# Kernel tuning notes

Measured on AMD Instinct MI355X. Metric: run time of the kernel, lower is better.

## Reference

```python
import jax, jax.numpy as jnp
import numpy as np

N_NODES = 100000
N_EDGES = 1600000
IN_DIM = 128
OUT_DIM = 16
HEADS = 4
NEG_SLOPE = 0.2


def setup_inputs() -> dict:
    key = jax.random.key(0)
    k1, k2, k3, k4, k5, k6, k7 = jax.random.split(key, 7)
    feat = jax.random.normal(k1, (N_NODES, IN_DIM), dtype=jnp.float32)
    src = jax.random.randint(k2, (N_EDGES,), 0, N_NODES, dtype=jnp.int32)
    dst = jax.random.randint(k3, (N_EDGES,), 0, N_NODES, dtype=jnp.int32)
    # Xavier-ish init for learned params (as in dgl GATConv)
    W = jax.random.normal(k4, (IN_DIM, HEADS * OUT_DIM), dtype=jnp.float32) / np.sqrt(IN_DIM)
    attn_l = jax.random.normal(k5, (HEADS, OUT_DIM), dtype=jnp.float32) / np.sqrt(OUT_DIM)
    attn_r = jax.random.normal(k6, (HEADS, OUT_DIM), dtype=jnp.float32) / np.sqrt(OUT_DIM)
    bias = jnp.zeros((HEADS * OUT_DIM,), dtype=jnp.float32)
    return {"feat": feat, "W": W, "attn_l": attn_l, "attn_r": attn_r,
            "bias": bias, "src": src, "dst": dst}


def reference(feat, W, attn_l, attn_r, bias, src, dst):
    N = feat.shape[0]
    H, D = attn_l.shape
    # Linear projection: [N, H, D]
    h = (feat @ W).reshape(N, H, D)
    # Per-node attention halves: [N, H]
    el = jnp.sum(h * attn_l[None], axis=-1)
    er = jnp.sum(h * attn_r[None], axis=-1)
    # Per-edge logits with LeakyReLU: [E, H]
    e = jax.nn.leaky_relu(el[src] + er[dst], negative_slope=NEG_SLOPE)
    # Segment softmax over incoming edges of each destination node
    e_max = jax.ops.segment_max(e, dst, num_segments=N)  # [N, H]
    ex = jnp.exp(e - e_max[dst])
    denom = jax.ops.segment_sum(ex, dst, num_segments=N)  # [N, H]
    alpha = ex / denom[dst]  # [E, H]
    # Scatter-weighted aggregation of source features
    msg = h[src] * alpha[:, :, None]  # [E, H, D]
    out = jax.ops.segment_sum(msg, dst, num_segments=N)  # [N, H, D]
    return out + bias.reshape(1, H, D)
```

## Files before the change

### kernel.cpp

```cpp
#include <hip/hip_runtime.h>
#include <math.h>

#define N_NODES 100000
#define N_EDGES 1600000
#define IN_DIM  128
#define HD      64
#define HEADS   4
#define ODIM    16
#define NEG_SLOPE 0.2f

#define BSH 8
#define NB  ((N_NODES + 255) >> 8)
#define PART_BLOCKS 256
#define EPB ((N_EDGES + PART_BLOCKS - 1) / PART_BLOCKS)
#define MAT (NB * PART_BLOCKS)
#define CAP 12288

__device__ inline unsigned short f32_to_bf16_rne(float f) {
    unsigned int b = __float_as_uint(f);
    b += 0x7FFFu + ((b >> 16) & 1u);
    return (unsigned short)(b >> 16);
}
__device__ inline float bf16_to_f32(unsigned short u) {
    return __uint_as_float(((unsigned int)u) << 16);
}

__global__ __launch_bounds__(256) void k_gemm_fused(const float* __restrict__ feat,
                                                    const float* __restrict__ W,
                                                    const float* __restrict__ attn_l,
                                                    const float* __restrict__ attn_r,
                                                    unsigned short* __restrict__ hbf,
                                                    float* __restrict__ el,
                                                    float* __restrict__ er) {
    __shared__ float sFT[32][132];
    __shared__ float sW[32][64];

    const int tid  = threadIdx.x;
    const int nid  = tid >> 4;
    const int cid  = tid & 15;
    const int c0   = cid * 4;
    const int nblk = blockIdx.x * 128;

    const int ln  = tid & 127;
    const int lkq = tid >> 7;

    float acc[8][4] = {};

    for (int kc = 0; kc < 4; ++kc) {
        const int k0 = kc * 32;
        const int gn = nblk + ln;
        #pragma unroll
        for (int i = 0; i < 4; ++i) {
            float4 v = (gn < N_NODES)
                ? *(const float4*)&feat[(size_t)gn * IN_DIM + k0 + lkq * 16 + i * 4]
                : make_float4(0.f, 0.f, 0.f, 0.f);
            const int kk = lkq * 16 + i * 4;
            sFT[kk + 0][ln] = v.x;
            sFT[kk + 1][ln] = v.y;
            sFT[kk + 2][ln] = v.z;
            sFT[kk + 3][ln] = v.w;
        }
        {
            const float4* W4 = (const float4*)(W + k0 * HD);
            float4 a = W4[tid];
            float4 b = W4[tid + 256];
            ((float4*)&sW[0][0])[tid]       = a;
            ((float4*)&sW[0][0])[tid + 256] = b;
        }
        __syncthreads();

        #pragma unroll 8
        for (int k = 0; k < 32; ++k) {
            float4 w  = *(const float4*)&sW[k][c0];
            float4 fA = *(const float4*)&sFT[k][nid * 8];
            float4 fB = *(const float4*)&sFT[k][nid * 8 + 4];
            float fr[8] = {fA.x, fA.y, fA.z, fA.w, fB.x, fB.y, fB.z, fB.w};
            #pragma unroll
            for (int r = 0; r < 8; ++r) {
                acc[r][0] = fmaf(fr[r], w.x, acc[r][0]);
                acc[r][1] = fmaf(fr[r], w.y, acc[r][1]);
                acc[r][2] = fmaf(fr[r], w.z, acc[r][2]);
                acc[r][3] = fmaf(fr[r], w.w, acc[r][3]);
            }
        }
        __syncthreads();
    }

    float4 al = *(const float4*)&attn_l[c0];
    float4 ar = *(const float4*)&attn_r[c0];
    const int head = cid >> 2;
    #pragma unroll
    for (int r = 0; r < 8; ++r) {
        int gn = nblk + nid * 8 + r;
        float pl = acc[r][0]*al.x + acc[r][1]*al.y + acc[r][2]*al.z + acc[r][3]*al.w;
        float pr = acc[r][0]*ar.x + acc[r][1]*ar.y + acc[r][2]*ar.z + acc[r][3]*ar.w;
        pl += __shfl_xor(pl, 1); pl += __shfl_xor(pl, 2);
        pr += __shfl_xor(pr, 1); pr += __shfl_xor(pr, 2);
        if (gn < N_NODES) {
            ushort4 hv;
            hv.x = f32_to_bf16_rne(acc[r][0]);
            hv.y = f32_to_bf16_rne(acc[r][1]);
            hv.z = f32_to_bf16_rne(acc[r][2]);
            hv.w = f32_to_bf16_rne(acc[r][3]);
            *(ushort4*)&hbf[(size_t)gn * HD + c0] = hv;
            if ((cid & 3) == 0) {
                el[gn * HEADS + head] = pl;
                er[gn * HEADS + head] = pr;
            }
        }
    }
}

__global__ __launch_bounds__(256) void k_count(const int* __restrict__ dst,
                                               int* __restrict__ counts) {
    __shared__ int h[NB];
    for (int i = threadIdx.x; i < NB; i += 256) h[i] = 0;
    __syncthreads();
    int beg = blockIdx.x * EPB;
    int end = beg + EPB; if (end > N_EDGES) end = N_EDGES;
    for (int e = beg + threadIdx.x; e < end; e += 256)
        atomicAdd(&h[dst[e] >> BSH], 1);
    __syncthreads();
    for (int i = threadIdx.x; i < NB; i += 256)
        counts[i * PART_BLOCKS + blockIdx.x] = h[i];
}

__global__ __launch_bounds__(256) void k_scanA(int* __restrict__ counts,
                                               int* __restrict__ bsums) {
    __shared__ int wsum[4];
    const int t = threadIdx.x;
    const int i = blockIdx.x * 256 + t;
    const int lane = t & 63, wv = t >> 6;
    int v = counts[i];
    int x = v;
    #pragma unroll
    for (int o = 1; o < 64; o <<= 1) {
        int u = __shfl_up(x, o);
        if (lane >= o) x += u;
    }
    if (lane == 63) wsum[wv] = x;
    __syncthreads();
    if (t == 0) {
        int r = 0;
        #pragma unroll
        for (int w = 0; w < 4; ++w) { int u = wsum[w]; wsum[w] = r; r += u; }
    }
    __syncthreads();
    int excl = x - v + wsum[wv];
    counts[i] = excl;
    if (t == 255) bsums[blockIdx.x] = excl + v;
}

__global__ __launch_bounds__(512) void k_scanB(int* __restrict__ bsums) {
    __shared__ int s[512];
    const int t = threadIdx.x;
    int v = (t < NB) ? bsums[t] : 0;
    s[t] = v;
    __syncthreads();
    for (int o = 1; o < 512; o <<= 1) {
        int u = (t >= o) ? s[t - o] : 0;
        __syncthreads();
        s[t] += u;
        __syncthreads();
    }
    if (t < NB) bsums[t] = s[t] - v;
}

__global__ __launch_bounds__(256) void k_partition(const int* __restrict__ src,
                                                   const int* __restrict__ dst,
                                                   const int* __restrict__ offs,
                                                   const int* __restrict__ bsums,
                                                   int* __restrict__ edges) {
    __shared__ int cur[NB];
    for (int i = threadIdx.x; i < NB; i += 256)
        cur[i] = offs[i * PART_BLOCKS + blockIdx.x] + bsums[i];
    __syncthreads();
    int beg = blockIdx.x * EPB;
    int end = beg + EPB; if (end > N_EDGES) end = N_EDGES;
    for (int e = beg + threadIdx.x; e < end; e += 256) {
        int d = dst[e];
        int pos = atomicAdd(&cur[d >> BSH], 1);
        edges[pos] = (int)(((unsigned)(d & 255) << 24) | (unsigned)src[e]);
    }
}

__global__ __launch_bounds__(256) void k_bucket_sort(const int* __restrict__ bsums,
                                                     int* __restrict__ edges,
                                                     int* __restrict__ deg_g,
                                                     int* __restrict__ cend_g) {
    __shared__ int stage[CAP];
    __shared__ int cnt[256];
    __shared__ int pos[256];
    __shared__ int wsum[4];
    const int b = blockIdx.x;
    const int t = threadIdx.x;
    const int base = bsums[b];
    const int bend = (b + 1 < NB) ? bsums[b + 1] : N_EDGES;
    int n = bend - base;
    if (n > CAP) n = CAP;

    for (int i = t; i < n; i += 256) stage[i] = edges[base + i];
    cnt[t] = 0;
    __syncthreads();
    for (int i = t; i < n; i += 256)
        atomicAdd(&cnt[((unsigned)stage[i]) >> 24], 1);
    __syncthreads();

    const int lane = t & 63, wv = t >> 6;
    int v = cnt[t];
    int x = v;
    #pragma unroll
    for (int o = 1; o < 64; o <<= 1) {
        int u = __shfl_up(x, o);
        if (lane >= o) x += u;
    }
    if (lane == 63) wsum[wv] = x;
    __syncthreads();
    if (t == 0) {
        int r = 0;
        #pragma unroll
        for (int w = 0; w < 4; ++w) { int u = wsum[w]; wsum[w] = r; r += u; }
    }
    __syncthreads();
    int excl = x - v + wsum[wv];
    pos[t] = excl;
    int node = (b << 8) + t;
    if (node < N_NODES) {
        deg_g[node]  = v;
        cend_g[node] = base + excl + v;
    }
    __syncthreads();

    for (int i = t; i < n; i += 256) {
        int e  = stage[i];
        int p  = atomicAdd(&pos[((unsigned)e) >> 24], 1);
        edges[base + p] = e & 0x00FFFFFF;
    }
}

#define NPW 4
__global__ __launch_bounds__(256) void k_aggregate_csr(
        const int* __restrict__ sorted_src,
        const int* __restrict__ cursor_end,
        const int* __restrict__ deg,
        const unsigned short* __restrict__ hbf,
        const float* __restrict__ el,
        const float* __restrict__ er,
        const float* __restrict__ bias,
        float* __restrict__ out) {
    const int wave = threadIdx.x >> 6;
    const int lane = threadIdx.x & 63;
    const int n0   = (blockIdx.x * 4 + wave) * NPW;
    if (n0 >= N_NODES) return;

    const int h1   = lane & 3;
    const int slot = lane >> 2;
    const int g    = lane >> 5;
    const int c    = lane & 31;
    const int hd   = c >> 3;

    int   endv[NPW], j0[NPW];
    float er1[NPW];
    float l_p[NPW];
    float accL[NPW], accH[NPW];

    #pragma unroll
    for (int k = 0; k < NPW; ++k) {
        int nk = n0 + k;
        bool ok = nk < N_NODES;
        endv[k] = ok ? cursor_end[nk] : 0;
        int dn  = ok ? deg[nk] : 0;
        j0[k]   = endv[k] - dn;
        er1[k]  = ok ? er[nk * HEADS + h1] : 0.f;
        l_p[k] = 0.f;
        accL[k] = 0.f; accH[k] = 0.f;
    }

    for (;;) {
        bool any = false;
        #pragma unroll
        for (int k = 0; k < NPW; ++k) any |= (j0[k] < endv[k]);
        if (!any) break;

        int   sK[NPW];
        float pK[NPW];
        #pragma unroll
        for (int k = 0; k < NPW; ++k) {
            int j = j0[k] + slot;
            sK[k] = (j0[k] < endv[k] && j < endv[k]) ? sorted_src[j] : -1;
        }
        #pragma unroll
        for (int k = 0; k < NPW; ++k) {
            if (sK[k] >= 0) {
                float t = el[sK[k] * HEADS + h1] + er1[k];
                t = t > 0.f ? t : NEG_SLOPE * t;
                pK[k] = __expf(t);
            } else {
                pK[k] = 0.f;
            }
        }
        #pragma unroll
        for (int k = 0; k < NPW; ++k) {
            if (j0[k] >= endv[k]) continue;
            float cs = pK[k];
            cs += __shfl_xor(cs, 4);
            cs += __shfl_xor(cs, 8);
            cs += __shfl_xor(cs, 16);
            cs += __shfl_xor(cs, 32);
            l_p[k] += cs;
        }
        #pragma unroll
        for (int k = 0; k < NPW; ++k) {
            if (j0[k] >= endv[k]) continue;
            float pe[8];
            unsigned off[8];
            #pragma unroll
            for (int t = 0; t < 8; ++t) {
                int e = 2 * t + g;
                pe[t] = __shfl(pK[k], e * 4 + hd);
                int se = __shfl(sK[k], e * 4);
                unsigned row = (se < 0) ? 0u : (unsigned)se;
                off[t] = row * HD + 2 * c;
            }
            unsigned u[8];
            #pragma unroll
            for (int t = 0; t < 8; ++t)
                u[t] = *(const unsigned*)&hbf[off[t]];
            #pragma unroll
            for (int t = 0; t < 8; ++t) {
                accL[k] = fmaf(pe[t], bf16_to_f32((unsigned short)(u[t] & 0xffffu)), accL[k]);
                accH[k] = fmaf(pe[t], bf16_to_f32((unsigned short)(u[t] >> 16)),     accH[k]);
            }
            j0[k] += 16;
        }
    }

    const float2 bl = ((const float2*)bias)[c];
    #pragma unroll
    for (int k = 0; k < NPW; ++k) {
        int nk = n0 + k;
        if (nk >= N_NODES) continue;
        float l   = __shfl(l_p[k], hd);
        float inv = (l > 0.f) ? 1.f / l : 0.f;
        float vL = accL[k] + __shfl_xor(accL[k], 32);
        float vH = accH[k] + __shfl_xor(accH[k], 32);
        if (lane < 32) {
            float2 v = make_float2(vL * inv + bl.x, vH * inv + bl.y);
            *(float2*)&out[nk * HD + 2 * c] = v;
        }
    }
}

extern "C" void kernel_launch(void* const* d_in, const int* in_sizes, int n_in,
                              void* d_out, int out_size, void* d_ws, size_t ws_size,
                              hipStream_t stream) {
    const float* feat   = (const float*)d_in[0];
    const float* W      = (const float*)d_in[1];
    const float* attn_l = (const float*)d_in[2];
    const float* attn_r = (const float*)d_in[3];
    const float* bias   = (const float*)d_in[4];
    const int*   src    = (const int*)d_in[5];
    const int*   dst    = (const int*)d_in[6];
    float* out = (float*)d_out;

    unsigned short* hbf = (unsigned short*)d_ws;
    float* el    = (float*)(hbf + (size_t)N_NODES * HD);
    float* er    = el + (size_t)N_NODES * HEADS;
    int*   deg    = (int*)(er + (size_t)N_NODES * HEADS);
    int*   cend   = deg + N_NODES;
    int*   edges  = cend + N_NODES;
    int*   counts = edges + N_EDGES;
    int*   bsums  = counts + MAT;

    k_gemm_fused<<<(N_NODES + 127) / 128, 256, 0, stream>>>(feat, W, attn_l, attn_r,
                                                            hbf, el, er);
    k_count<<<PART_BLOCKS, 256, 0, stream>>>(dst, counts);
    k_scanA<<<NB, 256, 0, stream>>>(counts, bsums);
    k_scanB<<<1, 512, 0, stream>>>(bsums);
    k_partition<<<PART_BLOCKS, 256, 0, stream>>>(src, dst, counts, bsums, edges);
    k_bucket_sort<<<NB, 256, 0, stream>>>(bsums, edges, deg, cend);
    const int nodes_per_block = 4 * NPW;
    k_aggregate_csr<<<(N_NODES + nodes_per_block - 1) / nodes_per_block, 256, 0, stream>>>(
        edges, cend, deg, hbf, el, er, bias, out);
}
```

Measured before the change: 240.7 us.

## Fuse bucket sort into aggregation and merge count into GEMM launch

```diff
diff --git a/kernel.cpp b/kernel.cpp
--- a/kernel.cpp
+++ b/kernel.cpp
@@ -9,12 +9,13 @@
 #define ODIM    16
 #define NEG_SLOPE 0.2f
 
-#define BSH 8
-#define NB  ((N_NODES + 255) >> 8)
+#define BSH 6
+#define NB  1563
 #define PART_BLOCKS 256
 #define EPB ((N_EDGES + PART_BLOCKS - 1) / PART_BLOCKS)
 #define MAT (NB * PART_BLOCKS)
-#define CAP 12288
+#define CAP2 1536
+#define G_GEMM ((N_NODES + 127) / 128)
 
 __device__ inline unsigned short f32_to_bf16_rne(float f) {
     unsigned int b = __float_as_uint(f);
@@ -25,104 +26,107 @@
     return __uint_as_float(((unsigned int)u) << 16);
 }
 
-__global__ __launch_bounds__(256) void k_gemm_fused(const float* __restrict__ feat,
+__global__ __launch_bounds__(256) void k_gemm_count(const float* __restrict__ feat,
                                                     const float* __restrict__ W,
                                                     const float* __restrict__ attn_l,
                                                     const float* __restrict__ attn_r,
+                                                    const int* __restrict__ dst,
                                                     unsigned short* __restrict__ hbf,
                                                     float* __restrict__ el,
-                                                    float* __restrict__ er) {
-    __shared__ float sFT[32][132];
-    __shared__ float sW[32][64];
-
-    const int tid  = threadIdx.x;
-    const int nid  = tid >> 4;
-    const int cid  = tid & 15;
-    const int c0   = cid * 4;
-    const int nblk = blockIdx.x * 128;
-
-    const int ln  = tid & 127;
-    const int lkq = tid >> 7;
-
-    float acc[8][4] = {};
-
-    for (int kc = 0; kc < 4; ++kc) {
-        const int k0 = kc * 32;
-        const int gn = nblk + ln;
-        #pragma unroll
-        for (int i = 0; i < 4; ++i) {
-            float4 v = (gn < N_NODES)
-                ? *(const float4*)&feat[(size_t)gn * IN_DIM + k0 + lkq * 16 + i * 4]
-                : make_float4(0.f, 0.f, 0.f, 0.f);
-            const int kk = lkq * 16 + i * 4;
-            sFT[kk + 0][ln] = v.x;
-            sFT[kk + 1][ln] = v.y;
-            sFT[kk + 2][ln] = v.z;
-            sFT[kk + 3][ln] = v.w;
-        }
-        {
-            const float4* W4 = (const float4*)(W + k0 * HD);
-            float4 a = W4[tid];
-            float4 b = W4[tid + 256];
-            ((float4*)&sW[0][0])[tid]       = a;
-            ((float4*)&sW[0][0])[tid + 256] = b;
-        }
+                                                    float* __restrict__ er,
+                                                    int* __restrict__ counts) {
+    __shared__ __align__(16) char smem[25088];
+    const int tid = threadIdx.x;
+
+    if (blockIdx.x < G_GEMM) {
+        float (*sFT)[132] = (float (*)[132])smem;
+        float (*sW)[64]   = (float (*)[64])(smem + 16896);
+
+        const int nid  = tid >> 4;
+        const int cid  = tid & 15;
+        const int c0   = cid * 4;
+        const int nblk = blockIdx.x * 128;
+        const int ln   = tid & 127;
+        const int lkq  = tid >> 7;
+
+        float acc[8][4] = {};
+
+        for (int kc = 0; kc < 4; ++kc) {
+            const int k0 = kc * 32;
+            const int gn = nblk + ln;
+            #pragma unroll
+            for (int i = 0; i < 4; ++i) {
+                float4 v = (gn < N_NODES)
+                    ? *(const float4*)&feat[(size_t)gn * IN_DIM + k0 + lkq * 16 + i * 4]
+                    : make_float4(0.f, 0.f, 0.f, 0.f);
+                const int kk = lkq * 16 + i * 4;
+                sFT[kk + 0][ln] = v.x;
+                sFT[kk + 1][ln] = v.y;
+                sFT[kk + 2][ln] = v.z;
+                sFT[kk + 3][ln] = v.w;
+            }
+            {
+                const float4* W4 = (const float4*)(W + k0 * HD);
+                float4 a = W4[tid];
+                float4 b = W4[tid + 256];
+                ((float4*)&sW[0][0])[tid]       = a;
+                ((float4*)&sW[0][0])[tid + 256] = b;
+            }
+            __syncthreads();
+
+            #pragma unroll 8
+            for (int k = 0; k < 32; ++k) {
+                float4 w  = *(const float4*)&sW[k][c0];
+                float4 fA = *(const float4*)&sFT[k][nid * 8];
+                float4 fB = *(const float4*)&sFT[k][nid * 8 + 4];
+                float fr[8] = {fA.x, fA.y, fA.z, fA.w, fB.x, fB.y, fB.z, fB.w};
+                #pragma unroll
+                for (int r = 0; r < 8; ++r) {
+                    acc[r][0] = fmaf(fr[r], w.x, acc[r][0]);
+                    acc[r][1] = fmaf(fr[r], w.y, acc[r][1]);
+                    acc[r][2] = fmaf(fr[r], w.z, acc[r][2]);
+                    acc[r][3] = fmaf(fr[r], w.w, acc[r][3]);
+                }
+            }
+            __syncthreads();
+        }
+
+        float4 al = *(const float4*)&attn_l[c0];
+        float4 ar = *(const float4*)&attn_r[c0];
+        const int head = cid >> 2;
+        #pragma unroll
+        for (int r = 0; r < 8; ++r) {
+            int gn = nblk + nid * 8 + r;
+            float pl = acc[r][0]*al.x + acc[r][1]*al.y + acc[r][2]*al.z + acc[r][3]*al.w;
+            float pr = acc[r][0]*ar.x + acc[r][1]*ar.y + acc[r][2]*ar.z + acc[r][3]*ar.w;
+            pl += __shfl_xor(pl, 1); pl += __shfl_xor(pl, 2);
+            pr += __shfl_xor(pr, 1); pr += __shfl_xor(pr, 2);
+            if (gn < N_NODES) {
+                ushort4 hv;
+                hv.x = f32_to_bf16_rne(acc[r][0]);
+                hv.y = f32_to_bf16_rne(acc[r][1]);
+                hv.z = f32_to_bf16_rne(acc[r][2]);
+                hv.w = f32_to_bf16_rne(acc[r][3]);
+                *(ushort4*)&hbf[(size_t)gn * HD + c0] = hv;
+                if ((cid & 3) == 0) {
+                    el[gn * HEADS + head] = pl;
+                    er[gn * HEADS + head] = pr;
+                }
+            }
+        }
+    } else {
+        int* hcnt = (int*)smem;
+        const int cb = blockIdx.x - G_GEMM;
+        for (int i = tid; i < NB; i += 256) hcnt[i] = 0;
         __syncthreads();
-
-        #pragma unroll 8
-        for (int k = 0; k < 32; ++k) {
-            float4 w  = *(const float4*)&sW[k][c0];
-            float4 fA = *(const float4*)&sFT[k][nid * 8];
-            float4 fB = *(const float4*)&sFT[k][nid * 8 + 4];
-            float fr[8] = {fA.x, fA.y, fA.z, fA.w, fB.x, fB.y, fB.z, fB.w};
-            #pragma unroll
-            for (int r = 0; r < 8; ++r) {
-                acc[r][0] = fmaf(fr[r], w.x, acc[r][0]);
-                acc[r][1] = fmaf(fr[r], w.y, acc[r][1]);
-                acc[r][2] = fmaf(fr[r], w.z, acc[r][2]);
-                acc[r][3] = fmaf(fr[r], w.w, acc[r][3]);
-            }
-        }
+        int beg = cb * EPB;
+        int end = beg + EPB; if (end > N_EDGES) end = N_EDGES;
+        for (int e = beg + tid; e < end; e += 256)
+            atomicAdd(&hcnt[dst[e] >> BSH], 1);
         __syncthreads();
-    }
-
-    float4 al = *(const float4*)&attn_l[c0];
-    float4 ar = *(const float4*)&attn_r[c0];
-    const int head = cid >> 2;
-    #pragma unroll
-    for (int r = 0; r < 8; ++r) {
-        int gn = nblk + nid * 8 + r;
-        float pl = acc[r][0]*al.x + acc[r][1]*al.y + acc[r][2]*al.z + acc[r][3]*al.w;
-        float pr = acc[r][0]*ar.x + acc[r][1]*ar.y + acc[r][2]*ar.z + acc[r][3]*ar.w;
-        pl += __shfl_xor(pl, 1); pl += __shfl_xor(pl, 2);
-        pr += __shfl_xor(pr, 1); pr += __shfl_xor(pr, 2);
-        if (gn < N_NODES) {
-            ushort4 hv;
-            hv.x = f32_to_bf16_rne(acc[r][0]);
-            hv.y = f32_to_bf16_rne(acc[r][1]);
-            hv.z = f32_to_bf16_rne(acc[r][2]);
-            hv.w = f32_to_bf16_rne(acc[r][3]);
-            *(ushort4*)&hbf[(size_t)gn * HD + c0] = hv;
-            if ((cid & 3) == 0) {
-                el[gn * HEADS + head] = pl;
-                er[gn * HEADS + head] = pr;
-            }
-        }
-    }
-}
-
-__global__ __launch_bounds__(256) void k_count(const int* __restrict__ dst,
-                                               int* __restrict__ counts) {
-    __shared__ int h[NB];
-    for (int i = threadIdx.x; i < NB; i += 256) h[i] = 0;
-    __syncthreads();
-    int beg = blockIdx.x * EPB;
-    int end = beg + EPB; if (end > N_EDGES) end = N_EDGES;
-    for (int e = beg + threadIdx.x; e < end; e += 256)
-        atomicAdd(&h[dst[e] >> BSH], 1);
-    __syncthreads();
-    for (int i = threadIdx.x; i < NB; i += 256)
-        counts[i * PART_BLOCKS + blockIdx.x] = h[i];
+        for (int i = tid; i < NB; i += 256)
+            counts[i * PART_BLOCKS + cb] = hcnt[i];
+    }
 }
 
 __global__ __launch_bounds__(256) void k_scanA(int* __restrict__ counts,
@@ -151,19 +155,23 @@
     if (t == 255) bsums[blockIdx.x] = excl + v;
 }
 
-__global__ __launch_bounds__(512) void k_scanB(int* __restrict__ bsums) {
-    __shared__ int s[512];
+__global__ __launch_bounds__(1024) void k_scanB(int* __restrict__ bsums) {
+    __shared__ int s[1024];
     const int t = threadIdx.x;
-    int v = (t < NB) ? bsums[t] : 0;
+    int v0 = (2 * t     < NB) ? bsums[2 * t]     : 0;
+    int v1 = (2 * t + 1 < NB) ? bsums[2 * t + 1] : 0;
+    int v = v0 + v1;
     s[t] = v;
     __syncthreads();
-    for (int o = 1; o < 512; o <<= 1) {
+    for (int o = 1; o < 1024; o <<= 1) {
         int u = (t >= o) ? s[t - o] : 0;
         __syncthreads();
         s[t] += u;
         __syncthreads();
     }
-    if (t < NB) bsums[t] = s[t] - v;
+    int run = s[t] - v;
+    if (2 * t < NB)     bsums[2 * t]     = run;
+    if (2 * t + 1 < NB) bsums[2 * t + 1] = run + v0;
 }
 
 __global__ __launch_bounds__(256) void k_partition(const int* __restrict__ src,
@@ -180,173 +188,154 @@
     for (int e = beg + threadIdx.x; e < end; e += 256) {
         int d = dst[e];
         int pos = atomicAdd(&cur[d >> BSH], 1);
-        edges[pos] = (int)(((unsigned)(d & 255) << 24) | (unsigned)src[e]);
-    }
-}
-
-__global__ __launch_bounds__(256) void k_bucket_sort(const int* __restrict__ bsums,
-                                                     int* __restrict__ edges,
-                                                     int* __restrict__ deg_g,
-                                                     int* __restrict__ cend_g) {
-    __shared__ int stage[CAP];
-    __shared__ int cnt[256];
-    __shared__ int pos[256];
-    __shared__ int wsum[4];
-    const int b = blockIdx.x;
-    const int t = threadIdx.x;
-    const int base = bsums[b];
-    const int bend = (b + 1 < NB) ? bsums[b + 1] : N_EDGES;
-    int n = bend - base;
-    if (n > CAP) n = CAP;
-
-    for (int i = t; i < n; i += 256) stage[i] = edges[base + i];
-    cnt[t] = 0;
-    __syncthreads();
-    for (int i = t; i < n; i += 256)
-        atomicAdd(&cnt[((unsigned)stage[i]) >> 24], 1);
-    __syncthreads();
-
-    const int lane = t & 63, wv = t >> 6;
-    int v = cnt[t];
-    int x = v;
-    #pragma unroll
-    for (int o = 1; o < 64; o <<= 1) {
-        int u = __shfl_up(x, o);
-        if (lane >= o) x += u;
-    }
-    if (lane == 63) wsum[wv] = x;
-    __syncthreads();
-    if (t == 0) {
-        int r = 0;
-        #pragma unroll
-        for (int w = 0; w < 4; ++w) { int u = wsum[w]; wsum[w] = r; r += u; }
-    }
-    __syncthreads();
-    int excl = x - v + wsum[wv];
-    pos[t] = excl;
-    int node = (b << 8) + t;
-    if (node < N_NODES) {
-        deg_g[node]  = v;
-        cend_g[node] = base + excl + v;
-    }
-    __syncthreads();
-
-    for (int i = t; i < n; i += 256) {
-        int e  = stage[i];
-        int p  = atomicAdd(&pos[((unsigned)e) >> 24], 1);
-        edges[base + p] = e & 0x00FFFFFF;
+        edges[pos] = (int)(((unsigned)(d & 63) << 24) | (unsigned)src[e]);
     }
 }
 
 #define NPW 4
-__global__ __launch_bounds__(256) void k_aggregate_csr(
-        const int* __restrict__ sorted_src,
-        const int* __restrict__ cursor_end,
-        const int* __restrict__ deg,
+__global__ __launch_bounds__(256) void k_sort_aggregate(
+        const int* __restrict__ edges,
+        const int* __restrict__ bsums,
         const unsigned short* __restrict__ hbf,
         const float* __restrict__ el,
         const float* __restrict__ er,
         const float* __restrict__ bias,
         float* __restrict__ out) {
-    const int wave = threadIdx.x >> 6;
-    const int lane = threadIdx.x & 63;
-    const int n0   = (blockIdx.x * 4 + wave) * NPW;
-    if (n0 >= N_NODES) return;
-
+    __shared__ int raw[CAP2];
+    __shared__ int sorted[CAP2];
+    __shared__ int cnt[64];
+    __shared__ int nstart[65];
+
+    const int b = blockIdx.x;
+    const int t = threadIdx.x;
+    const int base = bsums[b];
+    const int bend = (b + 1 < NB) ? bsums[b + 1] : N_EDGES;
+    int n = bend - base; if (n > CAP2) n = CAP2;
+
+    if (t < 64) cnt[t] = 0;
+    __syncthreads();
+    for (int i = t; i < n; i += 256) {
+        int e = edges[base + i];
+        raw[i] = e;
+        atomicAdd(&cnt[((unsigned)e) >> 24], 1);
+    }
+    __syncthreads();
+    if (t < 64) {
+        int v = cnt[t];
+        int x = v;
+        #pragma unroll
+        for (int o = 1; o < 64; o <<= 1) {
+            int u = __shfl_up(x, o);
+            if (t >= o) x += u;
+        }
+        nstart[t] = x - v;
+        if (t == 63) nstart[64] = x;
+        cnt[t] = x - v;
+    }
+    __syncthreads();
+    for (int i = t; i < n; i += 256) {
+        int e = raw[i];
+        int p = atomicAdd(&cnt[((unsigned)e) >> 24], 1);
+        sorted[p] = e & 0x00FFFFFF;
+    }
+    __syncthreads();
+
+    const int wave = t >> 6;
+    const int lane = t & 63;
     const int h1   = lane & 3;
     const int slot = lane >> 2;
     const int g    = lane >> 5;
     const int c    = lane & 31;
     const int hd   = c >> 3;
-
-    int   endv[NPW], j0[NPW];
-    float er1[NPW];
-    float l_p[NPW];
-    float accL[NPW], accH[NPW];
-
-    #pragma unroll
-    for (int k = 0; k < NPW; ++k) {
-        int nk = n0 + k;
-        bool ok = nk < N_NODES;
-        endv[k] = ok ? cursor_end[nk] : 0;
-        int dn  = ok ? deg[nk] : 0;
-        j0[k]   = endv[k] - dn;
-        er1[k]  = ok ? er[nk * HEADS + h1] : 0.f;
-        l_p[k] = 0.f;
-        accL[k] = 0.f; accH[k] = 0.f;
-    }
-
-    for (;;) {
-        bool any = false;
-        #pragma unroll
-        for (int k = 0; k < NPW; ++k) any |= (j0[k] < endv[k]);
-        if (!any) break;
-
-        int   sK[NPW];
-        float pK[NPW];
+    const float2 bl = ((const float2*)bias)[c];
+
+    for (int it = 0; it < 4; ++it) {
+        const int ln0 = wave * 16 + it * 4;
+        const int n0  = (b << 6) + ln0;
+
+        int   endv[NPW], j0[NPW];
+        float er1[NPW], l_p[NPW], accL[NPW], accH[NPW];
         #pragma unroll
         for (int k = 0; k < NPW; ++k) {
-            int j = j0[k] + slot;
-            sK[k] = (j0[k] < endv[k] && j < endv[k]) ? sorted_src[j] : -1;
-        }
+            int nk = n0 + k;
+            bool ok = (nk < N_NODES);
+            endv[k] = ok ? nstart[ln0 + k + 1] : 0;
+            j0[k]   = ok ? nstart[ln0 + k]     : 0;
+            er1[k]  = ok ? er[nk * HEADS + h1] : 0.f;
+            l_p[k] = 0.f; accL[k] = 0.f; accH[k] = 0.f;
+        }
+
+        for (;;) {
+            bool any = false;
+            #pragma unroll
+            for (int k = 0; k < NPW; ++k) any |= (j0[k] < endv[k]);
+            if (!any) break;
+
+            int   sK[NPW];
+            float pK[NPW];
+            #pragma unroll
+            for (int k = 0; k < NPW; ++k) {
+                int j = j0[k] + slot;
+                sK[k] = (j0[k] < endv[k] && j < endv[k]) ? sorted[j] : -1;
+            }
+            #pragma unroll
+            for (int k = 0; k < NPW; ++k) {
+                if (sK[k] >= 0) {
+                    float x = el[sK[k] * HEADS + h1] + er1[k];
+                    x = x > 0.f ? x : NEG_SLOPE * x;
+                    pK[k] = __expf(x);
+                } else {
+                    pK[k] = 0.f;
+                }
+            }
+            #pragma unroll
+            for (int k = 0; k < NPW; ++k) {
+                if (j0[k] >= endv[k]) continue;
+                float cs = pK[k];
+                cs += __shfl_xor(cs, 4);
+                cs += __shfl_xor(cs, 8);
+                cs += __shfl_xor(cs, 16);
+                cs += __shfl_xor(cs, 32);
+                l_p[k] += cs;
+            }
+            #pragma unroll
+            for (int k = 0; k < NPW; ++k) {
+                if (j0[k] >= endv[k]) continue;
+                float pe[8];
+                unsigned off[8];
+                #pragma unroll
+                for (int q = 0; q < 8; ++q) {
+                    int e = 2 * q + g;
+                    pe[q] = __shfl(pK[k], e * 4 + hd);
+                    int se = __shfl(sK[k], e * 4);
+                    unsigned row = (se < 0) ? 0u : (unsigned)se;
+                    off[q] = row * HD + 2 * c;
+                }
+                unsigned u[8];
+                #pragma unroll
+                for (int q = 0; q < 8; ++q)
+                    u[q] = *(const unsigned*)&hbf[off[q]];
+                #pragma unroll
+                for (int q = 0; q < 8; ++q) {
+                    accL[k] = fmaf(pe[q], bf16_to_f32((unsigned short)(u[q] & 0xffffu)), accL[k]);
+                    accH[k] = fmaf(pe[q], bf16_to_f32((unsigned short)(u[q] >> 16)),     accH[k]);
+                }
+                j0[k] += 16;
+            }
+        }
+
         #pragma unroll
         for (int k = 0; k < NPW; ++k) {
-            if (sK[k] >= 0) {
-                float t = el[sK[k] * HEADS + h1] + er1[k];
-                t = t > 0.f ? t : NEG_SLOPE * t;
-                pK[k] = __expf(t);
-            } else {
-                pK[k] = 0.f;
-            }
-        }
-        #pragma unroll
-        for (int k = 0; k < NPW; ++k) {
-            if (j0[k] >= endv[k]) continue;
-            float cs = pK[k];
-            cs += __shfl_xor(cs, 4);
-            cs += __shfl_xor(cs, 8);
-            cs += __shfl_xor(cs, 16);
-            cs += __shfl_xor(cs, 32);
-            l_p[k] += cs;
-        }
-        #pragma unroll
-        for (int k = 0; k < NPW; ++k) {
-            if (j0[k] >= endv[k]) continue;
-            float pe[8];
-            unsigned off[8];
-            #pragma unroll
-            for (int t = 0; t < 8; ++t) {
-                int e = 2 * t + g;
-                pe[t] = __shfl(pK[k], e * 4 + hd);
-                int se = __shfl(sK[k], e * 4);
-                unsigned row = (se < 0) ? 0u : (unsigned)se;
-                off[t] = row * HD + 2 * c;
-            }
-            unsigned u[8];
-            #pragma unroll
-            for (int t = 0; t < 8; ++t)
-                u[t] = *(const unsigned*)&hbf[off[t]];
-            #pragma unroll
-            for (int t = 0; t < 8; ++t) {
-                accL[k] = fmaf(pe[t], bf16_to_f32((unsigned short)(u[t] & 0xffffu)), accL[k]);
-                accH[k] = fmaf(pe[t], bf16_to_f32((unsigned short)(u[t] >> 16)),     accH[k]);
-            }
-            j0[k] += 16;
-        }
-    }
-
-    const float2 bl = ((const float2*)bias)[c];
-    #pragma unroll
-    for (int k = 0; k < NPW; ++k) {
-        int nk = n0 + k;
-        if (nk >= N_NODES) continue;
-        float l   = __shfl(l_p[k], hd);
-        float inv = (l > 0.f) ? 1.f / l : 0.f;
-        float vL = accL[k] + __shfl_xor(accL[k], 32);
-        float vH = accH[k] + __shfl_xor(accH[k], 32);
-        if (lane < 32) {
-            float2 v = make_float2(vL * inv + bl.x, vH * inv + bl.y);
-            *(float2*)&out[nk * HD + 2 * c] = v;
+            int nk = n0 + k;
+            if (nk >= N_NODES) continue;
+            float l   = __shfl(l_p[k], hd);
+            float inv = (l > 0.f) ? 1.f / l : 0.f;
+            float vL = accL[k] + __shfl_xor(accL[k], 32);
+            float vH = accH[k] + __shfl_xor(accH[k], 32);
+            if (lane < 32) {
+                float2 v = make_float2(vL * inv + bl.x, vH * inv + bl.y);
+                *(float2*)&out[nk * HD + 2 * c] = v;
+            }
         }
     }
 }
@@ -366,20 +355,14 @@
     unsigned short* hbf = (unsigned short*)d_ws;
     float* el    = (float*)(hbf + (size_t)N_NODES * HD);
     float* er    = el + (size_t)N_NODES * HEADS;
-    int*   deg    = (int*)(er + (size_t)N_NODES * HEADS);
-    int*   cend   = deg + N_NODES;
-    int*   edges  = cend + N_NODES;
+    int*   edges  = (int*)(er + (size_t)N_NODES * HEADS);
     int*   counts = edges + N_EDGES;
     int*   bsums  = counts + MAT;
 
-    k_gemm_fused<<<(N_NODES + 127) / 128, 256, 0, stream>>>(feat, W, attn_l, attn_r,
-                                                            hbf, el, er);
-    k_count<<<PART_BLOCKS, 256, 0, stream>>>(dst, counts);
+    k_gemm_count<<<G_GEMM + PART_BLOCKS, 256, 0, stream>>>(feat, W, attn_l, attn_r,
+                                                           dst, hbf, el, er, counts);
     k_scanA<<<NB, 256, 0, stream>>>(counts, bsums);
-    k_scanB<<<1, 512, 0, stream>>>(bsums);
+    k_scanB<<<1, 1024, 0, stream>>>(bsums);
     k_partition<<<PART_BLOCKS, 256, 0, stream>>>(src, dst, counts, bsums, edges);
-    k_bucket_sort<<<NB, 256, 0, stream>>>(bsums, edges, deg, cend);
-    const int nodes_per_block = 4 * NPW;
-    k_aggregate_csr<<<(N_NODES + nodes_per_block - 1) / nodes_per_block, 256, 0, stream>>>(
-        edges, cend, deg, hbf, el, er, bias, out);
-}
+    k_sort_aggregate<<<NB, 256, 0, stream>>>(edges, bsums, hbf, el, er, bias, out);
+}
```

New measurement: 251.7 us. 4.6% more time.
